# Kernel tuning notes

Measured on AMD Instinct MI355X. Metric: run time of the kernel, lower is better.

Reference implementation:

```python
import jax, jax.numpy as jnp
import numpy as np

N = 62          # EEG channels (nodes per graph)
B = 512         # graphs in batch
K = 2           # SGConv propagation steps
F_IN = 128
H = 64
C = 3


def _complete_graph_edge_index():
    # edge e = g*N*N + i*N + j connects node g*N+i -> g*N+j,
    # matching edge_weight = Wsym.reshape(-1).repeat(B) ordering.
    base = np.arange(N)
    ii = np.tile(np.repeat(base, N), B)
    jj = np.tile(np.tile(base, N), B)
    off = np.repeat(np.arange(B) * N, N * N)
    return jnp.asarray(np.stack([off + ii, off + jj]).astype(np.int32))


def setup_inputs() -> dict:
    key = jax.random.key(0)
    ks = jax.random.split(key, 6)
    n_total = B * N
    x = jax.random.normal(ks[0], (n_total, F_IN), dtype=jnp.float32)
    edge_weight_tril = jax.random.normal(ks[1], (N * (N + 1) // 2,), dtype=jnp.float32)
    W1 = jax.random.normal(ks[2], (H, F_IN), dtype=jnp.float32) * (1.0 / np.sqrt(F_IN))
    b1 = jax.random.normal(ks[3], (H,), dtype=jnp.float32) * 0.01
    W2 = jax.random.normal(ks[4], (C, H), dtype=jnp.float32) * (1.0 / np.sqrt(H))
    b2 = jax.random.normal(ks[5], (C,), dtype=jnp.float32) * 0.01
    edge_index = _complete_graph_edge_index()
    batch = jnp.asarray(np.repeat(np.arange(B), N).astype(np.int32))
    return {"x": x, "edge_weight_tril": edge_weight_tril, "W1": W1, "b1": b1,
            "W2": W2, "b2": b2, "edge_index": edge_index, "batch": batch,
            "batch_size": B}


def reference(x, edge_weight_tril, W1, b1, W2, b2, edge_index, batch, batch_size):
    n_total = x.shape[0]
    # rebuild symmetric dense adjacency from lower-tri params
    xs, ys = np.tril_indices(N)
    Wm = jnp.zeros((N, N), dtype=x.dtype).at[xs, ys].set(edge_weight_tril)
    Wsym = Wm + Wm.T - jnp.diag(jnp.diag(Wm))
    ew = jnp.tile(Wsym.reshape(-1), batch_size)            # [B*N*N]

    row, col = edge_index[0], edge_index[1]
    # symmetric normalization (graph already contains self loops)
    deg = jax.ops.segment_sum(jnp.abs(ew), row, num_segments=n_total)
    dinv = jnp.where(deg > 0, deg ** -0.5, 0.0)
    norm = dinv[row] * ew * dinv[col]                      # [E]

    # K-step SGConv propagation: gather, scale, scatter-add
    h = x
    for _ in range(K):
        h = jax.ops.segment_sum(norm[:, None] * h[row], col, num_segments=n_total)

    h = jax.nn.relu(h @ W1.T + b1)                         # [n_total, H]
    pooled = jax.ops.segment_sum(h, batch, num_segments=batch_size)  # global_add_pool
    latent_v = pooled                                      # dropout in eval mode = identity
    logits = latent_v @ W2.T + b2
    logp = jax.nn.log_softmax(logits, axis=-1)
    return latent_v, logp
```

## Files before the change

### kernel.cpp

```cpp
#include <hip/hip_runtime.h>
#include <math.h>

#define NN  62
#define BGR 512
#define FIN 128
#define HD  64
#define NC  3

typedef __attribute__((ext_vector_type(8))) short          bf16x8;
typedef __attribute__((ext_vector_type(4))) float          f32x4;
typedef __attribute__((ext_vector_type(4))) unsigned short us4;

static __device__ __forceinline__ unsigned short f2bf(float f) {
    union { float f; unsigned u; } v; v.f = f;
    unsigned u = v.u;
    return (unsigned short)((u + 0x7fffu + ((u >> 16) & 1u)) >> 16);
}
static __device__ __forceinline__ float bf2f(unsigned short h) {
    union { unsigned u; float f; } v; v.u = ((unsigned)h) << 16;
    return v.f;
}

__global__ __launch_bounds__(256) void gcn_all(
    const float* __restrict__ x, const float* __restrict__ tril,
    const float* __restrict__ W1, const float* __restrict__ b1,
    const float* __restrict__ W2, const float* __restrict__ b2,
    float* __restrict__ out) {
    __shared__ unsigned short SH[35840];
    __shared__ float TAIL[1088 + 64 + 64];
    float* partial = TAIL;
    float* b1S     = TAIL + 1088;
    float* dinvS   = TAIL + 1152;

    const int t = threadIdx.x;
    const int g = blockIdx.x;
    const int lane = t & 63, wv = t >> 6, quad = lane >> 4, l15 = lane & 15;

    if (t < 16) *(float4*)&b1S[4 * t] = ((const float4*)b1)[t];

    {
        const float4* w14 = (const float4*)W1;
        for (int e = t; e < 2048; e += 256) {
            int h = e >> 5, f4 = e & 31;
            float4 v = w14[e];
            us4 hh, ll;
            hh[0] = f2bf(v.x); ll[0] = f2bf(v.x - bf2f(hh[0]));
            hh[1] = f2bf(v.y); ll[1] = f2bf(v.y - bf2f(hh[1]));
            hh[2] = f2bf(v.z); ll[2] = f2bf(v.z - bf2f(hh[2]));
            hh[3] = f2bf(v.w); ll[3] = f2bf(v.w - bf2f(hh[3]));
            *(us4*)&SH[       h * 136 + f4 * 4] = hh;
            *(us4*)&SH[8704 + h * 136 + f4 * 4] = ll;
        }
    }

    bf16x8 xh[4], xl[4];
    {
        const int xr = 16 * wv + l15;
        if (xr < NN) {
            const float* xrow = x + (size_t)g * NN * FIN + (size_t)xr * FIN + quad * 8;
#pragma unroll
            for (int c = 0; c < 4; ++c) {
                float4 a = *(const float4*)(xrow + c * 32);
                float4 b = *(const float4*)(xrow + c * 32 + 4);
                float vv[8] = {a.x, a.y, a.z, a.w, b.x, b.y, b.z, b.w};
#pragma unroll
                for (int k = 0; k < 8; ++k) {
                    unsigned short h = f2bf(vv[k]);
                    xh[c][k] = (short)h;
                    xl[c][k] = (short)f2bf(vv[k] - bf2f(h));
                }
            }
        } else {
            bf16x8 zv = {0, 0, 0, 0, 0, 0, 0, 0};
#pragma unroll
            for (int c = 0; c < 4; ++c) { xh[c] = zv; xl[c] = zv; }
        }
    }

    const int arow_i = 16 * wv + l15;
    const int jbase  = 16 * quad;
    float wreg[16];
    float dinv_r;
    {
        float ps = 0.f;
#pragma unroll
        for (int jj = 0; jj < 16; ++jj) {
            int j = jbase + jj;
            float w = 0.f;
            if (arow_i < NN && j < NN) {
                int hi = arow_i > j ? arow_i : j;
                int lo = arow_i > j ? j : arow_i;
                w = tril[hi * (hi + 1) / 2 + lo];
            }
            wreg[jj] = w;
            ps += fabsf(w);
        }
        ps += __shfl_xor(ps, 16);
        ps += __shfl_xor(ps, 32);
        dinv_r = (ps > 0.f) ? (1.0f / sqrtf(ps)) : 0.f;
        if (lane < 16) dinvS[16 * wv + lane] = dinv_r;
    }
    __syncthreads();

    {
        const float di = dinv_r;
#pragma unroll
        for (int k = 0; k < 4; ++k) {
            float4 d4 = *(float4*)&dinvS[jbase + 4 * k];
            float dja[4] = {d4.x, d4.y, d4.z, d4.w};
            us4 hh, ll;
#pragma unroll
            for (int e = 0; e < 4; ++e) {
                float v = di * wreg[4 * k + e] * dja[e];
                hh[e] = f2bf(v);
                ll[e] = f2bf(v - bf2f(hh[e]));
            }
            *(us4*)&SH[17408 + arow_i * 72 + jbase + 4 * k] = hh;
            *(us4*)&SH[22016 + arow_i * 72 + jbase + 4 * k] = ll;
        }
    }
    __syncthreads();

    f32x4 za0 = {0,0,0,0}, za1 = {0,0,0,0}, za2 = {0,0,0,0}, za3 = {0,0,0,0};
    {
        const int arow = 17408 + (16 * wv + l15) * 72 + quad * 8;
#pragma unroll
        for (int c = 0; c < 2; ++c) {
            bf16x8 ahi = *(bf16x8*)&SH[arow + c * 32];
            bf16x8 alo = *(bf16x8*)&SH[4608 + arow + c * 32];
#define ATILE(ACC, NT) { \
            int bo = 17408 + (16 * NT + l15) * 72 + quad * 8 + c * 32; \
            bf16x8 bhi = *(bf16x8*)&SH[bo]; \
            bf16x8 blo = *(bf16x8*)&SH[4608 + bo]; \
            ACC = __builtin_amdgcn_mfma_f32_16x16x32_bf16(ahi, bhi, ACC, 0, 0, 0); \
            ACC = __builtin_amdgcn_mfma_f32_16x16x32_bf16(ahi, blo, ACC, 0, 0, 0); \
            ACC = __builtin_amdgcn_mfma_f32_16x16x32_bf16(alo, bhi, ACC, 0, 0, 0); }
            ATILE(za0, 0) ATILE(za1, 1) ATILE(za2, 2) ATILE(za3, 3)
#undef ATILE
        }
    }

    f32x4 y0 = {0,0,0,0}, y1 = {0,0,0,0}, y2 = {0,0,0,0}, y3 = {0,0,0,0};
    {
#pragma unroll
        for (int c = 0; c < 4; ++c) {
            bf16x8 ahi = xh[c];
            bf16x8 alo = xl[c];
#define P1TILE(ACC, NT) { \
            int bo = (16 * NT + l15) * 136 + quad * 8 + c * 32; \
            bf16x8 bhi = *(bf16x8*)&SH[bo]; \
            bf16x8 blo = *(bf16x8*)&SH[8704 + bo]; \
            ACC = __builtin_amdgcn_mfma_f32_16x16x32_bf16(ahi, bhi, ACC, 0, 0, 0); \
            ACC = __builtin_amdgcn_mfma_f32_16x16x32_bf16(ahi, blo, ACC, 0, 0, 0); \
            ACC = __builtin_amdgcn_mfma_f32_16x16x32_bf16(alo, bhi, ACC, 0, 0, 0); }
            P1TILE(y0, 0) P1TILE(y1, 1) P1TILE(y2, 2) P1TILE(y3, 3)
#undef P1TILE
        }
    }
    __syncthreads();

    {
        const int mbase = 16 * wv + quad * 4;
#define SPLITW(ACC, NT, HIOFF, LOOFF) { \
        int n = 16 * NT + l15; \
        us4 hh, ll; \
        hh[0] = f2bf(ACC[0]); ll[0] = f2bf(ACC[0] - bf2f(hh[0])); \
        hh[1] = f2bf(ACC[1]); ll[1] = f2bf(ACC[1] - bf2f(hh[1])); \
        hh[2] = f2bf(ACC[2]); ll[2] = f2bf(ACC[2] - bf2f(hh[2])); \
        hh[3] = f2bf(ACC[3]); ll[3] = f2bf(ACC[3] - bf2f(hh[3])); \
        *(us4*)&SH[(HIOFF) + n * 72 + mbase] = hh; \
        *(us4*)&SH[(LOOFF) + n * 72 + mbase] = ll; }
        SPLITW(y0, 0, 26624, 31232) SPLITW(y1, 1, 26624, 31232)
        SPLITW(y2, 2, 26624, 31232) SPLITW(y3, 3, 26624, 31232)
        SPLITW(za0, 0, 17408, 22016) SPLITW(za1, 1, 17408, 22016)
        SPLITW(za2, 2, 17408, 22016) SPLITW(za3, 3, 17408, 22016)
#undef SPLITW
    }
    __syncthreads();

    f32x4 z0 = {0,0,0,0}, z1 = {0,0,0,0}, z2 = {0,0,0,0}, z3 = {0,0,0,0};
    {
        const int arow = 17408 + (16 * wv + l15) * 72 + quad * 8;
#pragma unroll
        for (int c = 0; c < 2; ++c) {
            bf16x8 ahi = *(bf16x8*)&SH[arow + c * 32];
            bf16x8 alo = *(bf16x8*)&SH[4608 + arow + c * 32];
#define P2TILE(ACC, NT) { \
            int bo = 26624 + (16 * NT + l15) * 72 + quad * 8 + c * 32; \
            bf16x8 bhi = *(bf16x8*)&SH[bo]; \
            bf16x8 blo = *(bf16x8*)&SH[4608 + bo]; \
            ACC = __builtin_amdgcn_mfma_f32_16x16x32_bf16(ahi, bhi, ACC, 0, 0, 0); \
            ACC = __builtin_amdgcn_mfma_f32_16x16x32_bf16(ahi, blo, ACC, 0, 0, 0); \
            ACC = __builtin_amdgcn_mfma_f32_16x16x32_bf16(alo, bhi, ACC, 0, 0, 0); }
            P2TILE(z0, 0) P2TILE(z1, 1) P2TILE(z2, 2) P2TILE(z3, 3)
#undef P2TILE
        }
    }

    {
        const int mbase = 16 * wv + quad * 4;
        const int slot = 4 * wv + quad;
#define POOL(ACC, NT) { \
        int n = 16 * NT + l15; \
        float bn = b1S[n]; \
        float p = 0.f; \
        if (mbase + 0 < 62) p += fmaxf(ACC[0] + bn, 0.f); \
        if (mbase + 1 < 62) p += fmaxf(ACC[1] + bn, 0.f); \
        if (mbase + 2 < 62) p += fmaxf(ACC[2] + bn, 0.f); \
        if (mbase + 3 < 62) p += fmaxf(ACC[3] + bn, 0.f); \
        partial[n * 17 + slot] = p; }
        POOL(z0, 0) POOL(z1, 1) POOL(z2, 2) POOL(z3, 3)
#undef POOL
    }
    __syncthreads();

    if (t < HD) {
        float s = 0.f;
#pragma unroll
        for (int q = 0; q < 16; ++q) s += partial[t * 17 + q];
        out[(size_t)g * HD + t] = s;
        float l0 = s * W2[t];
        float l1 = s * W2[64 + t];
        float l2 = s * W2[128 + t];
#pragma unroll
        for (int off = 32; off > 0; off >>= 1) {
            l0 += __shfl_down(l0, off);
            l1 += __shfl_down(l1, off);
            l2 += __shfl_down(l2, off);
        }
        if (t == 0) {
            l0 += b2[0]; l1 += b2[1]; l2 += b2[2];
            float m = fmaxf(l0, fmaxf(l1, l2));
            float lse = m + logf(expf(l0 - m) + expf(l1 - m) + expf(l2 - m));
            float* lp = out + (size_t)BGR * HD + (size_t)g * NC;
            lp[0] = l0 - lse; lp[1] = l1 - lse; lp[2] = l2 - lse;
        }
    }
}

extern "C" void kernel_launch(void* const* d_in, const int* in_sizes, int n_in,
                              void* d_out, int out_size, void* d_ws, size_t ws_size,
                              hipStream_t stream) {
    const float* x    = (const float*)d_in[0];
    const float* tril = (const float*)d_in[1];
    const float* W1   = (const float*)d_in[2];
    const float* b1   = (const float*)d_in[3];
    const float* W2   = (const float*)d_in[4];
    const float* b2   = (const float*)d_in[5];
    float* out = (float*)d_out;

    gcn_all<<<BGR, 256, 0, stream>>>(x, tril, W1, b1, W2, b2, out);
}
```

Measured before the change: 95.24 us.

## Process two graphs per 512-thread block sharing W1 and normalized adjacency setup

Each block now handles two graphs with eight waves. The W1 bf16 split and the normalized adjacency construction are done once per block and divided between the two wave groups. The A·A product is also split so each half computes two of the four column tiles. This halves the redundant per-block setup of the graph-independent weights and A². In exchange it uses more LDS per block and launches half as many blocks, which may reduce occupancy or the number of CUs that get work.

```diff
diff --git a/kernel.cpp b/kernel.cpp
--- a/kernel.cpp
+++ b/kernel.cpp
@@ -21,26 +21,57 @@
     return v.f;
 }
 
-__global__ __launch_bounds__(256) void gcn_all(
+__global__ __launch_bounds__(512) void gcn_all(
     const float* __restrict__ x, const float* __restrict__ tril,
     const float* __restrict__ W1, const float* __restrict__ b1,
     const float* __restrict__ W2, const float* __restrict__ b2,
     float* __restrict__ out) {
-    __shared__ unsigned short SH[35840];
-    __shared__ float TAIL[1088 + 64 + 64];
+    __shared__ unsigned short SH[45056];
+    __shared__ float TAIL[2176 + 64 + 64];
     float* partial = TAIL;
-    float* b1S     = TAIL + 1088;
-    float* dinvS   = TAIL + 1152;
+    float* b1S     = TAIL + 2176;
+    float* dinvS   = TAIL + 2240;
 
     const int t = threadIdx.x;
-    const int g = blockIdx.x;
+    const int gb = blockIdx.x;
     const int lane = t & 63, wv = t >> 6, quad = lane >> 4, l15 = lane & 15;
+    const int w4 = wv & 3, gsel = wv >> 2;
+    const int graph = 2 * gb + gsel;
 
     if (t < 16) *(float4*)&b1S[4 * t] = ((const float4*)b1)[t];
 
-    {
+    bf16x8 xh[4], xl[4];
+    {
+        const int xr = 16 * w4 + l15;
+        if (xr < NN) {
+            const float* xrow = x + (size_t)graph * NN * FIN + (size_t)xr * FIN + quad * 8;
+#pragma unroll
+            for (int c = 0; c < 4; ++c) {
+                float4 a = *(const float4*)(xrow + c * 32);
+                float4 b = *(const float4*)(xrow + c * 32 + 4);
+                float vv[8] = {a.x, a.y, a.z, a.w, b.x, b.y, b.z, b.w};
+#pragma unroll
+                for (int k = 0; k < 8; ++k) {
+                    unsigned short h = f2bf(vv[k]);
+                    xh[c][k] = (short)h;
+                    xl[c][k] = (short)f2bf(vv[k] - bf2f(h));
+                }
+            }
+        } else {
+            bf16x8 zv = {0, 0, 0, 0, 0, 0, 0, 0};
+#pragma unroll
+            for (int c = 0; c < 4; ++c) { xh[c] = zv; xl[c] = zv; }
+        }
+    }
+
+    const int arow_i = 16 * w4 + l15;
+    const int jbase  = 16 * quad;
+    float wreg[16];
+    float dinv_r = 0.f;
+
+    if (gsel == 1) {
         const float4* w14 = (const float4*)W1;
-        for (int e = t; e < 2048; e += 256) {
+        for (int e = t - 256; e < 2048; e += 256) {
             int h = e >> 5, f4 = e & 31;
             float4 v = w14[e];
             us4 hh, ll;
@@ -51,37 +82,7 @@
             *(us4*)&SH[       h * 136 + f4 * 4] = hh;
             *(us4*)&SH[8704 + h * 136 + f4 * 4] = ll;
         }
-    }
-
-    bf16x8 xh[4], xl[4];
-    {
-        const int xr = 16 * wv + l15;
-        if (xr < NN) {
-            const float* xrow = x + (size_t)g * NN * FIN + (size_t)xr * FIN + quad * 8;
-#pragma unroll
-            for (int c = 0; c < 4; ++c) {
-                float4 a = *(const float4*)(xrow + c * 32);
-                float4 b = *(const float4*)(xrow + c * 32 + 4);
-                float vv[8] = {a.x, a.y, a.z, a.w, b.x, b.y, b.z, b.w};
-#pragma unroll
-                for (int k = 0; k < 8; ++k) {
-                    unsigned short h = f2bf(vv[k]);
-                    xh[c][k] = (short)h;
-                    xl[c][k] = (short)f2bf(vv[k] - bf2f(h));
-                }
-            }
-        } else {
-            bf16x8 zv = {0, 0, 0, 0, 0, 0, 0, 0};
-#pragma unroll
-            for (int c = 0; c < 4; ++c) { xh[c] = zv; xl[c] = zv; }
-        }
-    }
-
-    const int arow_i = 16 * wv + l15;
-    const int jbase  = 16 * quad;
-    float wreg[16];
-    float dinv_r;
-    {
+    } else {
         float ps = 0.f;
 #pragma unroll
         for (int jj = 0; jj < 16; ++jj) {
@@ -98,11 +99,11 @@
         ps += __shfl_xor(ps, 16);
         ps += __shfl_xor(ps, 32);
         dinv_r = (ps > 0.f) ? (1.0f / sqrtf(ps)) : 0.f;
-        if (lane < 16) dinvS[16 * wv + lane] = dinv_r;
-    }
-    __syncthreads();
-
-    {
+        if (lane < 16) dinvS[16 * w4 + lane] = dinv_r;
+    }
+    __syncthreads();
+
+    if (gsel == 0) {
         const float di = dinv_r;
 #pragma unroll
         for (int k = 0; k < 4; ++k) {
@@ -121,21 +122,22 @@
     }
     __syncthreads();
 
-    f32x4 za0 = {0,0,0,0}, za1 = {0,0,0,0}, za2 = {0,0,0,0}, za3 = {0,0,0,0};
-    {
-        const int arow = 17408 + (16 * wv + l15) * 72 + quad * 8;
+    f32x4 za0 = {0,0,0,0}, za1 = {0,0,0,0};
+    {
+        const int arow = 17408 + arow_i * 72 + quad * 8;
+        const int nt0 = 2 * gsel;
 #pragma unroll
         for (int c = 0; c < 2; ++c) {
             bf16x8 ahi = *(bf16x8*)&SH[arow + c * 32];
             bf16x8 alo = *(bf16x8*)&SH[4608 + arow + c * 32];
 #define ATILE(ACC, NT) { \
-            int bo = 17408 + (16 * NT + l15) * 72 + quad * 8 + c * 32; \
+            int bo = 17408 + (16 * (NT) + l15) * 72 + quad * 8 + c * 32; \
             bf16x8 bhi = *(bf16x8*)&SH[bo]; \
             bf16x8 blo = *(bf16x8*)&SH[4608 + bo]; \
             ACC = __builtin_amdgcn_mfma_f32_16x16x32_bf16(ahi, bhi, ACC, 0, 0, 0); \
             ACC = __builtin_amdgcn_mfma_f32_16x16x32_bf16(ahi, blo, ACC, 0, 0, 0); \
             ACC = __builtin_amdgcn_mfma_f32_16x16x32_bf16(alo, bhi, ACC, 0, 0, 0); }
-            ATILE(za0, 0) ATILE(za1, 1) ATILE(za2, 2) ATILE(za3, 3)
+            ATILE(za0, nt0) ATILE(za1, nt0 + 1)
 #undef ATILE
         }
     }
@@ -147,7 +149,7 @@
             bf16x8 ahi = xh[c];
             bf16x8 alo = xl[c];
 #define P1TILE(ACC, NT) { \
-            int bo = (16 * NT + l15) * 136 + quad * 8 + c * 32; \
+            int bo = (16 * (NT) + l15) * 136 + quad * 8 + c * 32; \
             bf16x8 bhi = *(bf16x8*)&SH[bo]; \
             bf16x8 blo = *(bf16x8*)&SH[8704 + bo]; \
             ACC = __builtin_amdgcn_mfma_f32_16x16x32_bf16(ahi, bhi, ACC, 0, 0, 0); \
@@ -159,10 +161,11 @@
     }
     __syncthreads();
 
-    {
-        const int mbase = 16 * wv + quad * 4;
+    const int ytbase = 26624 + gsel * 9216;
+    {
+        const int mbase = 16 * w4 + quad * 4;
 #define SPLITW(ACC, NT, HIOFF, LOOFF) { \
-        int n = 16 * NT + l15; \
+        int n = 16 * (NT) + l15; \
         us4 hh, ll; \
         hh[0] = f2bf(ACC[0]); ll[0] = f2bf(ACC[0] - bf2f(hh[0])); \
         hh[1] = f2bf(ACC[1]); ll[1] = f2bf(ACC[1] - bf2f(hh[1])); \
@@ -170,23 +173,23 @@
         hh[3] = f2bf(ACC[3]); ll[3] = f2bf(ACC[3] - bf2f(hh[3])); \
         *(us4*)&SH[(HIOFF) + n * 72 + mbase] = hh; \
         *(us4*)&SH[(LOOFF) + n * 72 + mbase] = ll; }
-        SPLITW(y0, 0, 26624, 31232) SPLITW(y1, 1, 26624, 31232)
-        SPLITW(y2, 2, 26624, 31232) SPLITW(y3, 3, 26624, 31232)
-        SPLITW(za0, 0, 17408, 22016) SPLITW(za1, 1, 17408, 22016)
-        SPLITW(za2, 2, 17408, 22016) SPLITW(za3, 3, 17408, 22016)
+        SPLITW(y0, 0, ytbase, ytbase + 4608) SPLITW(y1, 1, ytbase, ytbase + 4608)
+        SPLITW(y2, 2, ytbase, ytbase + 4608) SPLITW(y3, 3, ytbase, ytbase + 4608)
+        SPLITW(za0, 2 * gsel,     17408, 22016)
+        SPLITW(za1, 2 * gsel + 1, 17408, 22016)
 #undef SPLITW
     }
     __syncthreads();
 
     f32x4 z0 = {0,0,0,0}, z1 = {0,0,0,0}, z2 = {0,0,0,0}, z3 = {0,0,0,0};
     {
-        const int arow = 17408 + (16 * wv + l15) * 72 + quad * 8;
+        const int arow = 17408 + arow_i * 72 + quad * 8;
 #pragma unroll
         for (int c = 0; c < 2; ++c) {
             bf16x8 ahi = *(bf16x8*)&SH[arow + c * 32];
             bf16x8 alo = *(bf16x8*)&SH[4608 + arow + c * 32];
 #define P2TILE(ACC, NT) { \
-            int bo = 26624 + (16 * NT + l15) * 72 + quad * 8 + c * 32; \
+            int bo = ytbase + (16 * (NT) + l15) * 72 + quad * 8 + c * 32; \
             bf16x8 bhi = *(bf16x8*)&SH[bo]; \
             bf16x8 blo = *(bf16x8*)&SH[4608 + bo]; \
             ACC = __builtin_amdgcn_mfma_f32_16x16x32_bf16(ahi, bhi, ACC, 0, 0, 0); \
@@ -198,41 +201,47 @@
     }
 
     {
-        const int mbase = 16 * wv + quad * 4;
-        const int slot = 4 * wv + quad;
+        const int mbase = 16 * w4 + quad * 4;
+        const int slot = 4 * w4 + quad;
+        float* part = partial + gsel * 1088;
 #define POOL(ACC, NT) { \
-        int n = 16 * NT + l15; \
+        int n = 16 * (NT) + l15; \
         float bn = b1S[n]; \
         float p = 0.f; \
         if (mbase + 0 < 62) p += fmaxf(ACC[0] + bn, 0.f); \
         if (mbase + 1 < 62) p += fmaxf(ACC[1] + bn, 0.f); \
         if (mbase + 2 < 62) p += fmaxf(ACC[2] + bn, 0.f); \
         if (mbase + 3 < 62) p += fmaxf(ACC[3] + bn, 0.f); \
-        partial[n * 17 + slot] = p; }
+        part[n * 17 + slot] = p; }
         POOL(z0, 0) POOL(z1, 1) POOL(z2, 2) POOL(z3, 3)
 #undef POOL
     }
     __syncthreads();
 
-    if (t < HD) {
+    int tg = -1, tt = 0;
+    if (t < 64)                    { tg = 0; tt = t; }
+    else if (t >= 256 && t < 320)  { tg = 1; tt = t - 256; }
+    if (tg >= 0) {
+        const float* part = partial + tg * 1088;
+        const int gr = 2 * gb + tg;
         float s = 0.f;
 #pragma unroll
-        for (int q = 0; q < 16; ++q) s += partial[t * 17 + q];
-        out[(size_t)g * HD + t] = s;
-        float l0 = s * W2[t];
-        float l1 = s * W2[64 + t];
-        float l2 = s * W2[128 + t];
+        for (int q = 0; q < 16; ++q) s += part[tt * 17 + q];
+        out[(size_t)gr * HD + tt] = s;
+        float l0 = s * W2[tt];
+        float l1 = s * W2[64 + tt];
+        float l2 = s * W2[128 + tt];
 #pragma unroll
         for (int off = 32; off > 0; off >>= 1) {
             l0 += __shfl_down(l0, off);
             l1 += __shfl_down(l1, off);
             l2 += __shfl_down(l2, off);
         }
-        if (t == 0) {
+        if (tt == 0) {
             l0 += b2[0]; l1 += b2[1]; l2 += b2[2];
             float m = fmaxf(l0, fmaxf(l1, l2));
             float lse = m + logf(expf(l0 - m) + expf(l1 - m) + expf(l2 - m));
-            float* lp = out + (size_t)BGR * HD + (size_t)g * NC;
+            float* lp = out + (size_t)BGR * HD + (size_t)gr * NC;
             lp[0] = l0 - lse; lp[1] = l1 - lse; lp[2] = l2 - lse;
         }
     }
@@ -249,5 +258,5 @@
     const float* b2   = (const float*)d_in[5];
     float* out = (float*)d_out;
 
-    gcn_all<<<BGR, 256, 0, stream>>>(x, tril, W1, b1, W2, b2, out);
-}
+    gcn_all<<<BGR / 2, 512, 0, stream>>>(x, tril, W1, b1, W2, b2, out);
+}
```

Result: faster. 92.88 us (median of 2 runs) (-2.5%).
